# Kernel tuning notes

Hardware: AMD Instinct MI355X
Metric: run time of the kernel (lower is better)

## Reference

```python
import jax, jax.numpy as jnp
import numpy as np
import math

B, H, D, P, N = 65536, 256, 32, 16, 32768
LOG_C = math.log(math.sqrt(2.0 * math.pi))


def setup_inputs() -> dict:
    key = jax.random.key(0)
    ks = jax.random.split(key, 8)
    h = jax.random.normal(ks[0], (B, H), dtype=jnp.float32)
    p = jax.random.normal(ks[1], (B, 2 * D), dtype=jnp.float32)
    X_obs = jax.random.normal(ks[2], (N, D), dtype=jnp.float32)
    M_obs = (jax.random.uniform(ks[3], (N, D)) < 0.5).astype(jnp.float32)
    i_obs = jnp.arange(N, dtype=jnp.int32)  # unique indices into batch rows
    std = math.sqrt(2.0 / (4 + P))
    w_prep = std * jax.random.normal(ks[4], (D, 4, P), dtype=jnp.float32)
    bias_prep = 0.1 * jnp.ones((D, P), dtype=jnp.float32)
    # keras GRUCell params (reset_after=True): kernel [in,3H], recurrent [H,3H], two biases [3H]
    gru_kernel = 0.05 * jax.random.normal(ks[5], (P * D, 3 * H), dtype=jnp.float32)
    gru_rec_kernel = 0.05 * jax.random.normal(ks[6], (H, 3 * H), dtype=jnp.float32)
    gru_bias_in = jnp.zeros((3 * H,), dtype=jnp.float32)
    gru_bias_rec = jnp.zeros((3 * H,), dtype=jnp.float32)
    return {"h": h, "p": p, "X_obs": X_obs, "M_obs": M_obs, "i_obs": i_obs,
            "w_prep": w_prep, "bias_prep": bias_prep,
            "gru_kernel": gru_kernel, "gru_rec_kernel": gru_rec_kernel,
            "gru_bias_in": gru_bias_in, "gru_bias_rec": gru_bias_rec}


def _gru_cell(x, h_prev, kernel, rec_kernel, bias_in, bias_rec):
    # keras GRUCell, reset_after=True, tanh / sigmoid activations
    mx = x @ kernel + bias_in            # [N, 3H]
    mh = h_prev @ rec_kernel + bias_rec  # [N, 3H]
    xz, xr, xh = jnp.split(mx, 3, axis=1)
    rz, rr, rh = jnp.split(mh, 3, axis=1)
    z = jax.nn.sigmoid(xz + rz)
    r = jax.nn.sigmoid(xr + rr)
    hh = jnp.tanh(xh + r * rh)
    return z * h_prev + (1.0 - z) * hh


def reference(h, p, X_obs, M_obs, i_obs, w_prep, bias_prep,
              gru_kernel, gru_rec_kernel, gru_bias_in, gru_bias_rec):
    d, ph = w_prep.shape[0], w_prep.shape[2]
    p_obs = p[i_obs]                      # gather [N, 2D]
    mean, logvar = jnp.split(p_obs, 2, axis=1)
    sigma = jnp.exp(0.5 * logvar)
    error = (X_obs - mean) / sigma
    losses = 0.5 * ((error * error + logvar + 2.0 * LOG_C) * M_obs)  # [N, D]
    gi = jnp.stack([X_obs, mean, logvar, error], axis=2)             # [N, D, 4]
    gi = jnp.einsum('ndk,dkp->ndp', gi, w_prep) + bias_prep          # per-feature matmul
    gi = jax.nn.relu(gi)
    gi = jnp.transpose(gi, (2, 0, 1))                                # [P, N, D]
    gi = (gi * M_obs).reshape(-1, ph * d)                            # [N, P*D] (TF reshape semantics)
    h_obs = h[i_obs]
    h_new = _gru_cell(gi, h_obs, gru_kernel, gru_rec_kernel, gru_bias_in, gru_bias_rec)
    h_out = h.at[i_obs].set(h_new)                                   # scatter-update
    return (h_out, losses)
```

## Files before the change

kernel.cpp:

```cpp
#include <hip/hip_runtime.h>
#include <hip/hip_bf16.h>
#include <math.h>

#define NROWS 32768
#define DD 32
#define PPH 16
#define HH 256
#define BB 65536
#define TWO_LOG_C 1.8378770664093453f

typedef __attribute__((ext_vector_type(8))) __bf16 bf16x8;
typedef __attribute__((ext_vector_type(4))) float f32x4;
typedef unsigned int u32;

__device__ __forceinline__ float sigm_f(float x) { return 1.0f / (1.0f + __expf(-x)); }
__device__ __forceinline__ float tanh_f(float x) { return 1.0f - 2.0f / (1.0f + __expf(2.0f * x)); }

__device__ __forceinline__ void gl_lds16(const __bf16* g, __bf16* l) {
    __builtin_amdgcn_global_load_lds(
        (const __attribute__((address_space(1))) u32*)g,
        (__attribute__((address_space(3))) u32*)l, 16, 0, 0);
}

__global__ __launch_bounds__(256) void pre_kernel(
    const float* __restrict__ h,
    const float* __restrict__ p,
    const float* __restrict__ X_obs,
    const float* __restrict__ M_obs,
    const int*   __restrict__ i_obs,
    const float* __restrict__ w_prep,
    const float* __restrict__ bias_prep,
    const float* __restrict__ gk,
    const float* __restrict__ grk,
    float* __restrict__ losses,
    __bf16* __restrict__ G,
    __bf16* __restrict__ Hb,
    __bf16* __restrict__ Kt,
    __bf16* __restrict__ Rt,
    float* __restrict__ h_out)
{
    __shared__ float arena[4160];
    const int bid = blockIdx.x;
    const int tid = threadIdx.x;

    if (bid < 4096) {
        float (*w2)[33] = (float(*)[33])arena;
        float (*b2)[33] = (float(*)[33])(arena + 64 * 33);
        for (int i = tid; i < 2048; i += 256) w2[i & 63][i >> 6] = w_prep[i];
        for (int i = tid; i < 512; i += 256)  b2[i & 15][i >> 4] = bias_prep[i];
        __syncthreads();

        const int gid = bid * 256 + tid;
        const int n = gid >> 5;
        const int d = gid & 31;
        const int idx = i_obs[n];

        float mean   = p[idx * 64 + d];
        float logvar = p[idx * 64 + 32 + d];
        float x      = X_obs[gid];
        float m      = M_obs[gid];

        float inv_sigma = __expf(-0.5f * logvar);
        float err = (x - mean) * inv_sigma;
        losses[gid] = 0.5f * ((err * err + logvar + TWO_LOG_C) * m);

        #pragma unroll
        for (int q = 0; q < PPH; ++q) {
            float v = x      * w2[q][d]
                    + mean   * w2[16 + q][d]
                    + logvar * w2[32 + q][d]
                    + err    * w2[48 + q][d]
                    + b2[q][d];
            v = fmaxf(v, 0.0f) * m;
            G[(size_t)q * (NROWS * DD) + gid] = (__bf16)v;
        }

        const float* hsrc = h + (size_t)idx * 256 + d * 8;
        float4 a = ((const float4*)hsrc)[0];
        float4 b = ((const float4*)hsrc)[1];
        bf16x8 v8;
        v8[0] = (__bf16)a.x; v8[1] = (__bf16)a.y; v8[2] = (__bf16)a.z; v8[3] = (__bf16)a.w;
        v8[4] = (__bf16)b.x; v8[5] = (__bf16)b.y; v8[6] = (__bf16)b.z; v8[7] = (__bf16)b.w;
        *(bf16x8*)(Hb + (size_t)n * 256 + d * 8) = v8;

        const float4* hf4 = (const float4*)h;
        float4* of4 = (float4*)h_out;
        #pragma unroll
        for (int k2 = 0; k2 < 4; ++k2) {
            int i4 = gid + k2 * 1048576;
            of4[i4] = hf4[i4];
        }
    } else {
        float (*t)[65] = (float(*)[65])arena;
        int b = bid - 4096;
        const float* src; __bf16* dst; int K, k0, j0;
        if (b < 96) { src = gk;  dst = Kt; K = 512; k0 = (b & 7) * 64; j0 = (b >> 3) * 64; }
        else { b -= 96; src = grk; dst = Rt; K = 256; k0 = (b & 3) * 64; j0 = (b >> 2) * 64; }
        int tx = tid & 63, ty = tid >> 6;
        #pragma unroll
        for (int i = 0; i < 16; ++i) {
            int k = ty * 16 + i;
            t[k][tx] = src[(size_t)(k0 + k) * 768 + j0 + tx];
        }
        __syncthreads();
        #pragma unroll
        for (int i = 0; i < 16; ++i) {
            int j = ty * 16 + i;
            dst[(size_t)(j0 + j) * K + k0 + tx] = (__bf16)t[tx][j];
        }
    }
}

#define A_EL 4096
#define B_EL 6144

struct StageCtx {
    const __bf16 *G, *Hb, *Kt, *Rt;
    int i0, j0, wave, lane;
};

__device__ __forceinline__ void stage_step(int t, const StageCtx& c,
                                           __bf16* ldsA, __bf16* ldsB) {
    const bool ph1 = t < 16;
    const int k0 = (ph1 ? t : (t - 16)) * 32;
    const int Kd = ph1 ? 512 : 256;
    const __bf16* Asrc = ph1 ? c.G : c.Hb;
    const __bf16* Bsrc = ph1 ? c.Kt : c.Rt;
    __bf16* dA = ldsA + (t & 1) * A_EL;
    __bf16* dB = ldsB + (t & 1) * B_EL;
    const int rsub  = c.lane >> 2;
    const int sslot = c.lane & 3;
    #pragma unroll
    for (int s = 0; s < 5; ++s) {
        int u = c.wave * 5 + s;
        if (u < 8) {
            int row = u * 16 + rsub;
            int kg = sslot ^ ((row >> 1) & 3);
            gl_lds16(Asrc + (size_t)(c.i0 + row) * Kd + k0 + kg * 8,
                     dA + u * 512);
        } else {
            int v = u - 8;
            int br = v * 16 + rsub;
            int kg = sslot ^ ((br >> 1) & 3);
            int mat = br >> 6, jr = br & 63;
            gl_lds16(Bsrc + (size_t)(mat * 256 + c.j0 + jr) * Kd + k0 + kg * 8,
                     dB + v * 512);
        }
    }
}

__device__ __forceinline__ void compute_step(
    const __bf16* cA, const __bf16* cB,
    int kgrp, int lrow, int rw, int cw,
    f32x4 (&az)[4][2], f32x4 (&ar)[4][2], f32x4 (&ah)[4][2])
{
    bf16x8 af[4], bz[2], brf[2], bh[2];
    #pragma unroll
    for (int mt = 0; mt < 4; ++mt) {
        int r = rw * 64 + mt * 16 + lrow;
        af[mt] = *(const bf16x8*)(cA + r * 32 + (kgrp ^ ((r >> 1) & 3)) * 8);
    }
    #pragma unroll
    for (int jt = 0; jt < 2; ++jt) {
        int jj = cw * 32 + jt * 16 + lrow;
        int b0 = jj, b1 = 64 + jj, b2r = 128 + jj;
        bz[jt]  = *(const bf16x8*)(cB + b0  * 32 + (kgrp ^ ((b0  >> 1) & 3)) * 8);
        brf[jt] = *(const bf16x8*)(cB + b1  * 32 + (kgrp ^ ((b1  >> 1) & 3)) * 8);
        bh[jt]  = *(const bf16x8*)(cB + b2r * 32 + (kgrp ^ ((b2r >> 1) & 3)) * 8);
    }
    #pragma unroll
    for (int mt = 0; mt < 4; ++mt)
        #pragma unroll
        for (int jt = 0; jt < 2; ++jt) {
            az[mt][jt] = __builtin_amdgcn_mfma_f32_16x16x32_bf16(af[mt], bz[jt],  az[mt][jt], 0, 0, 0);
            ar[mt][jt] = __builtin_amdgcn_mfma_f32_16x16x32_bf16(af[mt], brf[jt], ar[mt][jt], 0, 0, 0);
            ah[mt][jt] = __builtin_amdgcn_mfma_f32_16x16x32_bf16(af[mt], bh[jt],  ah[mt][jt], 0, 0, 0);
        }
}

__global__ __launch_bounds__(256, 2) void gru_mfma_kernel(
    const __bf16* __restrict__ G,
    const __bf16* __restrict__ Hb,
    const float*  __restrict__ h,
    const int*    __restrict__ i_obs,
    const __bf16* __restrict__ Kt,
    const __bf16* __restrict__ Rt,
    const float*  __restrict__ bi,
    const float*  __restrict__ brc,
    float* __restrict__ h_out)
{
    __shared__ __bf16 ldsA[2][A_EL];
    __shared__ __bf16 ldsB[2][B_EL];
    __shared__ int idx_s[128];

    const int tid  = threadIdx.x;
    const int lane = tid & 63;
    const int wave = tid >> 6;
    const int lrow = lane & 15;
    const int kgrp = lane >> 4;
    const int rw = wave >> 1;
    const int cw = wave & 1;

    int bid = blockIdx.x;
    int swz = (bid & 7) * 128 + (bid >> 3);
    const int i0 = (swz >> 2) * 128;
    const int j0 = (swz & 3) * 64;

    if (tid < 128) idx_s[tid] = i_obs[i0 + tid];
    asm volatile("s_waitcnt lgkmcnt(0)" ::: "memory");

    f32x4 az[4][2], ar[4][2], axh[4][2], arh[4][2];
    const f32x4 zero4 = {0.f, 0.f, 0.f, 0.f};
    #pragma unroll
    for (int m = 0; m < 4; ++m)
        #pragma unroll
        for (int j = 0; j < 2; ++j) {
            az[m][j] = zero4; ar[m][j] = zero4; axh[m][j] = zero4; arh[m][j] = zero4;
        }

    StageCtx ctx{G, Hb, Kt, Rt, i0, j0, wave, lane};

    stage_step(0, ctx, &ldsA[0][0], &ldsB[0][0]);
    stage_step(1, ctx, &ldsA[0][0], &ldsB[0][0]);

    #pragma unroll
    for (int t = 0; t < 16; ++t) {
        asm volatile("s_waitcnt vmcnt(5)" ::: "memory");
        __builtin_amdgcn_s_barrier();
        compute_step(&ldsA[t & 1][0], &ldsB[t & 1][0], kgrp, lrow, rw, cw,
                     az, ar, axh);
        __builtin_amdgcn_s_barrier();
        stage_step(t + 2, ctx, &ldsA[0][0], &ldsB[0][0]);
    }
    #pragma unroll
    for (int t = 16; t < 24; ++t) {
        if (t < 23) { asm volatile("s_waitcnt vmcnt(5)" ::: "memory"); }
        else        { asm volatile("s_waitcnt vmcnt(0)" ::: "memory"); }
        __builtin_amdgcn_s_barrier();
        compute_step(&ldsA[t & 1][0], &ldsB[t & 1][0], kgrp, lrow, rw, cw,
                     az, ar, arh);
        __builtin_amdgcn_s_barrier();
        if (t + 2 < 24) stage_step(t + 2, ctx, &ldsA[0][0], &ldsB[0][0]);
    }

    #pragma unroll
    for (int mt = 0; mt < 4; ++mt) {
        int rl0 = rw * 64 + mt * 16 + kgrp * 4;
        #pragma unroll
        for (int jt = 0; jt < 2; ++jt) {
            int j = j0 + cw * 32 + jt * 16 + lrow;
            float b_z  = bi[j]       + brc[j];
            float b_r  = bi[256 + j] + brc[256 + j];
            float b_xh = bi[512 + j];
            float b_rh = brc[512 + j];
            #pragma unroll
            for (int r = 0; r < 4; ++r) {
                size_t hoff = (size_t)idx_s[rl0 + r] * 256 + j;
                float z  = sigm_f(az[mt][jt][r] + b_z);
                float rg = sigm_f(ar[mt][jt][r] + b_r);
                float hh = tanh_f(axh[mt][jt][r] + b_xh + rg * (arh[mt][jt][r] + b_rh));
                float hp = h[hoff];
                h_out[hoff] = z * hp + (1.0f - z) * hh;
            }
        }
    }
}

extern "C" void kernel_launch(void* const* d_in, const int* in_sizes, int n_in,
                              void* d_out, int out_size, void* d_ws, size_t ws_size,
                              hipStream_t stream) {
    const float* h         = (const float*)d_in[0];
    const float* p         = (const float*)d_in[1];
    const float* X_obs     = (const float*)d_in[2];
    const float* M_obs     = (const float*)d_in[3];
    const int*   i_obs     = (const int*)  d_in[4];
    const float* w_prep    = (const float*)d_in[5];
    const float* bias_prep = (const float*)d_in[6];
    const float* gk        = (const float*)d_in[7];
    const float* grk       = (const float*)d_in[8];
    const float* gbi       = (const float*)d_in[9];
    const float* gbr       = (const float*)d_in[10];

    float* out    = (float*)d_out;
    float* h_out  = out;
    float* losses = out + (size_t)BB * HH;

    char* ws = (char*)d_ws;
    __bf16* G  = (__bf16*)ws;
    __bf16* Kt = (__bf16*)(ws + 33554432);
    __bf16* Rt = (__bf16*)(ws + 34340864);
    __bf16* Hb = (__bf16*)(ws + 34734080);

    pre_kernel<<<4240, 256, 0, stream>>>(
        h, p, X_obs, M_obs, i_obs, w_prep, bias_prep, gk, grk,
        losses, G, Hb, Kt, Rt, h_out);

    gru_mfma_kernel<<<1024, 256, 0, stream>>>(
        G, Hb, h, i_obs, Kt, Rt, gbi, gbr, h_out);
}
```

Measured before the change: 218.5 us.

## Double K-step per pipeline stage and raise MFMA priority in GRU GEMM

```diff
diff --git a/kernel.cpp b/kernel.cpp
--- a/kernel.cpp
+++ b/kernel.cpp
@@ -111,71 +111,66 @@
     }
 }
 
-#define A_EL 4096
-#define B_EL 6144
-
-struct StageCtx {
-    const __bf16 *G, *Hb, *Kt, *Rt;
-    int i0, j0, wave, lane;
-};
-
-__device__ __forceinline__ void stage_step(int t, const StageCtx& c,
-                                           __bf16* ldsA, __bf16* ldsB) {
-    const bool ph1 = t < 16;
-    const int k0 = (ph1 ? t : (t - 16)) * 32;
-    const int Kd = ph1 ? 512 : 256;
-    const __bf16* Asrc = ph1 ? c.G : c.Hb;
-    const __bf16* Bsrc = ph1 ? c.Kt : c.Rt;
-    __bf16* dA = ldsA + (t & 1) * A_EL;
-    __bf16* dB = ldsB + (t & 1) * B_EL;
-    const int rsub  = c.lane >> 2;
-    const int sslot = c.lane & 3;
-    #pragma unroll
-    for (int s = 0; s < 5; ++s) {
-        int u = c.wave * 5 + s;
-        if (u < 8) {
-            int row = u * 16 + rsub;
-            int kg = sslot ^ ((row >> 1) & 3);
-            gl_lds16(Asrc + (size_t)(c.i0 + row) * Kd + k0 + kg * 8,
-                     dA + u * 512);
+#define A_BUF 8192
+#define B_BUF 12288
+
+__device__ __forceinline__ void stage(const __bf16* __restrict__ Asrc,
+                                      const __bf16* __restrict__ Bsrc,
+                                      int Kd, int i0, int j0, int koff,
+                                      int wave, int lane,
+                                      __bf16* dA, __bf16* dB) {
+    const int rsub = lane >> 3;
+    const int slot = lane & 7;
+    #pragma unroll
+    for (int s = 0; s < 10; ++s) {
+        int u = wave * 10 + s;
+        if (u < 16) {
+            int ra = u * 8 + rsub;
+            int xs = slot ^ (ra & 7);
+            gl_lds16(Asrc + (size_t)(i0 + ra) * Kd + koff + xs * 8, dA + u * 512);
         } else {
-            int v = u - 8;
-            int br = v * 16 + rsub;
-            int kg = sslot ^ ((br >> 1) & 3);
-            int mat = br >> 6, jr = br & 63;
-            gl_lds16(Bsrc + (size_t)(mat * 256 + c.j0 + jr) * Kd + k0 + kg * 8,
+            int v = u - 16;
+            int rb = v * 8 + rsub;
+            int xs = slot ^ (rb & 7);
+            int mat = rb >> 6, jr = rb & 63;
+            gl_lds16(Bsrc + (size_t)(mat * 256 + j0 + jr) * Kd + koff + xs * 8,
                      dB + v * 512);
         }
     }
 }
 
-__device__ __forceinline__ void compute_step(
-    const __bf16* cA, const __bf16* cB,
+__device__ __forceinline__ void compute(const __bf16* cA, const __bf16* cB,
     int kgrp, int lrow, int rw, int cw,
     f32x4 (&az)[4][2], f32x4 (&ar)[4][2], f32x4 (&ah)[4][2])
 {
-    bf16x8 af[4], bz[2], brf[2], bh[2];
-    #pragma unroll
-    for (int mt = 0; mt < 4; ++mt) {
-        int r = rw * 64 + mt * 16 + lrow;
-        af[mt] = *(const bf16x8*)(cA + r * 32 + (kgrp ^ ((r >> 1) & 3)) * 8);
-    }
-    #pragma unroll
-    for (int jt = 0; jt < 2; ++jt) {
-        int jj = cw * 32 + jt * 16 + lrow;
-        int b0 = jj, b1 = 64 + jj, b2r = 128 + jj;
-        bz[jt]  = *(const bf16x8*)(cB + b0  * 32 + (kgrp ^ ((b0  >> 1) & 3)) * 8);
-        brf[jt] = *(const bf16x8*)(cB + b1  * 32 + (kgrp ^ ((b1  >> 1) & 3)) * 8);
-        bh[jt]  = *(const bf16x8*)(cB + b2r * 32 + (kgrp ^ ((b2r >> 1) & 3)) * 8);
-    }
-    #pragma unroll
-    for (int mt = 0; mt < 4; ++mt)
+    #pragma unroll
+    for (int kk = 0; kk < 2; ++kk) {
+        const int sx = kk * 4 + kgrp;
+        const int x8 = (sx ^ (lrow & 7)) * 8;
+        bf16x8 af[4], bz[2], brf[2], bh[2];
+        #pragma unroll
+        for (int mt = 0; mt < 4; ++mt) {
+            int ra = rw * 64 + mt * 16 + lrow;
+            af[mt] = *(const bf16x8*)(cA + ra * 64 + x8);
+        }
         #pragma unroll
         for (int jt = 0; jt < 2; ++jt) {
-            az[mt][jt] = __builtin_amdgcn_mfma_f32_16x16x32_bf16(af[mt], bz[jt],  az[mt][jt], 0, 0, 0);
-            ar[mt][jt] = __builtin_amdgcn_mfma_f32_16x16x32_bf16(af[mt], brf[jt], ar[mt][jt], 0, 0, 0);
-            ah[mt][jt] = __builtin_amdgcn_mfma_f32_16x16x32_bf16(af[mt], bh[jt],  ah[mt][jt], 0, 0, 0);
-        }
+            int jr = cw * 32 + jt * 16 + lrow;
+            bz[jt]  = *(const bf16x8*)(cB + (jr)       * 64 + x8);
+            brf[jt] = *(const bf16x8*)(cB + (64 + jr)  * 64 + x8);
+            bh[jt]  = *(const bf16x8*)(cB + (128 + jr) * 64 + x8);
+        }
+        __builtin_amdgcn_s_setprio(1);
+        #pragma unroll
+        for (int mt = 0; mt < 4; ++mt)
+            #pragma unroll
+            for (int jt = 0; jt < 2; ++jt) {
+                az[mt][jt] = __builtin_amdgcn_mfma_f32_16x16x32_bf16(af[mt], bz[jt],  az[mt][jt], 0, 0, 0);
+                ar[mt][jt] = __builtin_amdgcn_mfma_f32_16x16x32_bf16(af[mt], brf[jt], ar[mt][jt], 0, 0, 0);
+                ah[mt][jt] = __builtin_amdgcn_mfma_f32_16x16x32_bf16(af[mt], bh[jt],  ah[mt][jt], 0, 0, 0);
+            }
+        __builtin_amdgcn_s_setprio(0);
+    }
 }
 
 __global__ __launch_bounds__(256, 2) void gru_mfma_kernel(
@@ -189,9 +184,8 @@
     const float*  __restrict__ brc,
     float* __restrict__ h_out)
 {
-    __shared__ __bf16 ldsA[2][A_EL];
-    __shared__ __bf16 ldsB[2][B_EL];
-    __shared__ int idx_s[128];
+    __shared__ __bf16 ldsA[2 * A_BUF];
+    __shared__ __bf16 ldsB[2 * B_BUF];
 
     const int tid  = threadIdx.x;
     const int lane = tid & 63;
@@ -206,9 +200,6 @@
     const int i0 = (swz >> 2) * 128;
     const int j0 = (swz & 3) * 64;
 
-    if (tid < 128) idx_s[tid] = i_obs[i0 + tid];
-    asm volatile("s_waitcnt lgkmcnt(0)" ::: "memory");
-
     f32x4 az[4][2], ar[4][2], axh[4][2], arh[4][2];
     const f32x4 zero4 = {0.f, 0.f, 0.f, 0.f};
     #pragma unroll
@@ -218,29 +209,35 @@
             az[m][j] = zero4; ar[m][j] = zero4; axh[m][j] = zero4; arh[m][j] = zero4;
         }
 
-    StageCtx ctx{G, Hb, Kt, Rt, i0, j0, wave, lane};
-
-    stage_step(0, ctx, &ldsA[0][0], &ldsB[0][0]);
-    stage_step(1, ctx, &ldsA[0][0], &ldsB[0][0]);
-
-    #pragma unroll
-    for (int t = 0; t < 16; ++t) {
-        asm volatile("s_waitcnt vmcnt(5)" ::: "memory");
-        __builtin_amdgcn_s_barrier();
-        compute_step(&ldsA[t & 1][0], &ldsB[t & 1][0], kgrp, lrow, rw, cw,
-                     az, ar, axh);
-        __builtin_amdgcn_s_barrier();
-        stage_step(t + 2, ctx, &ldsA[0][0], &ldsB[0][0]);
-    }
-    #pragma unroll
-    for (int t = 16; t < 24; ++t) {
-        if (t < 23) { asm volatile("s_waitcnt vmcnt(5)" ::: "memory"); }
-        else        { asm volatile("s_waitcnt vmcnt(0)" ::: "memory"); }
-        __builtin_amdgcn_s_barrier();
-        compute_step(&ldsA[t & 1][0], &ldsB[t & 1][0], kgrp, lrow, rw, cw,
-                     az, ar, arh);
-        __builtin_amdgcn_s_barrier();
-        if (t + 2 < 24) stage_step(t + 2, ctx, &ldsA[0][0], &ldsB[0][0]);
+    stage(G, Kt, 512, i0, j0, 0,  wave, lane, ldsA,         ldsB);
+    stage(G, Kt, 512, i0, j0, 64, wave, lane, ldsA + A_BUF, ldsB + B_BUF);
+
+    #pragma unroll
+    for (int t = 0; t < 8; ++t) {
+        asm volatile("s_waitcnt vmcnt(10)" ::: "memory");
+        __builtin_amdgcn_s_barrier();
+        compute(ldsA + (t & 1) * A_BUF, ldsB + (t & 1) * B_BUF,
+                kgrp, lrow, rw, cw, az, ar, axh);
+        __builtin_amdgcn_s_barrier();
+        int ns = t + 2;
+        if (ns < 8)
+            stage(G, Kt, 512, i0, j0, ns * 64, wave, lane,
+                  ldsA + (ns & 1) * A_BUF, ldsB + (ns & 1) * B_BUF);
+        else
+            stage(Hb, Rt, 256, i0, j0, (ns - 8) * 64, wave, lane,
+                  ldsA + (ns & 1) * A_BUF, ldsB + (ns & 1) * B_BUF);
+    }
+    #pragma unroll
+    for (int tp = 0; tp < 4; ++tp) {
+        if (tp < 3) { asm volatile("s_waitcnt vmcnt(10)" ::: "memory"); }
+        else        { asm volatile("s_waitcnt vmcnt(0)"  ::: "memory"); }
+        __builtin_amdgcn_s_barrier();
+        compute(ldsA + (tp & 1) * A_BUF, ldsB + (tp & 1) * B_BUF,
+                kgrp, lrow, rw, cw, az, ar, arh);
+        __builtin_amdgcn_s_barrier();
+        if (tp < 2)
+            stage(Hb, Rt, 256, i0, j0, (tp + 2) * 64, wave, lane,
+                  ldsA + (tp & 1) * A_BUF, ldsB + (tp & 1) * B_BUF);
     }
 
     #pragma unroll
@@ -255,7 +252,8 @@
             float b_rh = brc[512 + j];
             #pragma unroll
             for (int r = 0; r < 4; ++r) {
-                size_t hoff = (size_t)idx_s[rl0 + r] * 256 + j;
+                int idx = i_obs[i0 + rl0 + r];
+                size_t hoff = (size_t)idx * 256 + j;
                 float z  = sigm_f(az[mt][jt][r] + b_z);
                 float rg = sigm_f(ar[mt][jt][r] + b_r);
                 float hh = tanh_f(axh[mt][jt][r] + b_xh + rg * (arh[mt][jt][r] + b_rh));
```

Measured after the change: 219.5 us. Within noise of the previous version (+0.5%).
